# Kernel tuning notes

Hardware: AMD Instinct MI355X
Metric: run time of the kernel (lower is better)

Reference implementation:

```python
import jax, jax.numpy as jnp
import numpy as np

N, E = 100000, 1600000
FEATS, HIDDEN, CLASSES, DEPTH = 512, 64, 16, 10
EMB_DIM = 1 + int(np.log2(HIDDEN))   # 7
ADJ_H = 4 + EMB_DIM                  # 11
DIFF = 0.9


def setup_inputs() -> dict:
    key = jax.random.key(0)
    ks = jax.random.split(key, 8)
    return {
        "x": jax.random.normal(ks[0], (N, FEATS), jnp.float32),
        "edges": jax.random.randint(ks[1], (2, E), 0, N, jnp.int32),
        "W_dim": jax.random.normal(ks[2], (FEATS, HIDDEN), jnp.float32) / np.sqrt(FEATS),
        "b_dim": jnp.zeros((HIDDEN,), jnp.float32),
        "emb": jax.random.normal(ks[3], (HIDDEN, EMB_DIM), jnp.float32),
        "W_a1": jax.random.normal(ks[4], (2 + EMB_DIM, ADJ_H), jnp.float32) / np.sqrt(2 + EMB_DIM),
        "b_a1": jnp.zeros((ADJ_H,), jnp.float32),
        "W_a2": jax.random.normal(ks[5], (ADJ_H, 1), jnp.float32) / np.sqrt(ADJ_H),
        "b_a2": jnp.zeros((1,), jnp.float32),
        "W_cls": jax.random.normal(ks[6], (HIDDEN, CLASSES), jnp.float32) / np.sqrt(HIDDEN),
        "b_cls": jnp.zeros((CLASSES,), jnp.float32),
    }


def reference(x, edges, W_dim, b_dim, emb, W_a1, b_a1, W_a2, b_a2, W_cls, b_cls):
    n = x.shape[0]
    src, dst = edges[0], edges[1]
    # symmetric-normalized sparse aggregation (GCN-style GraphConv, cached norm)
    deg = jax.ops.segment_sum(jnp.ones(src.shape[0], x.dtype), dst, num_segments=n)
    dinv = jnp.where(deg > 0, jax.lax.rsqrt(jnp.maximum(deg, 1.0)), 0.0)
    wnorm = dinv[src] * dinv[dst]  # [E]

    def conv(h):  # [n, H] -> [n, H]
        return jax.ops.segment_sum(h[src] * wnorm[:, None], dst, num_segments=n)

    h = x @ W_dim + b_dim        # [n, HIDDEN]
    h0 = h
    for _ in range(DEPTH):       # personalized-PageRank-style diffusion
        h = conv(h) * DIFF + (1.0 - DIFF) * h0

    hdim = h.shape[1]
    xt = h.T.reshape(-1, 1)      # [HIDDEN*n, 1]
    h0t = h0.T.reshape(-1, 1)
    # class_indicator built after reshape(-1,1): num_classes = 1 -> all-zero indices
    e = jnp.broadcast_to(emb[0], (xt.shape[0], emb.shape[1]))  # [HIDDEN*n, EMB_DIM]
    f = jnp.concatenate([xt, h0t, e], axis=1)                  # [HIDDEN*n, 9]
    f = jax.nn.leaky_relu(f @ W_a1 + b_a1, negative_slope=0.01)
    f = (f @ W_a2 + b_a2) * 0.5                                # [HIDDEN*n, 1]
    h = f.reshape(hdim, n).T                                   # [n, HIDDEN]
    # dropout: eval mode -> no-op
    h0 = h
    for _ in range(DEPTH):
        h = conv(h) * DIFF + (1.0 - DIFF) * h0
    return h @ W_cls + b_cls     # [n, CLASSES]
```

## Files before the change

### kernel.cpp

```cpp
#include <hip/hip_runtime.h>
#include <hip/hip_bf16.h>
#include <hip/hip_fp16.h>
#include <stdint.h>

#define FEATS   512
#define HIDDEN  64
#define CLASSES 16
#define EMB_DIM 7
#define ADJ_H   11
#define DEPTH   10

typedef __hip_bfloat16 bf16;
typedef __attribute__((ext_vector_type(8))) short short8;
typedef __attribute__((ext_vector_type(4))) float f32x4;

__device__ __forceinline__ float b2f(bf16 v) { return __bfloat162float(v); }

__global__ void k_detect(const unsigned short* __restrict__ xs, int* __restrict__ flag) {
    __shared__ int cnt;
    if (threadIdx.x == 0) cnt = 0;
    __syncthreads();
    int c = 0;
    for (int i = threadIdx.x; i < 4096; i += 256) {
        unsigned e = (xs[i] >> 7) & 0xFFu;
        if (e >= 134u) c++;
    }
    atomicAdd(&cnt, c);
    __syncthreads();
    if (threadIdx.x == 0) *flag = (cnt < 64) ? 1 : 0;
}

__global__ __launch_bounds__(256) void k_deg(const int* __restrict__ edges,
                                             int* __restrict__ deg, int E) {
    int e = blockIdx.x * 256 + threadIdx.x;
    if (e < E) atomicAdd(&deg[edges[E + e]], 1);
}

__global__ __launch_bounds__(256) void k_scan1(const int* __restrict__ deg,
                                               int* __restrict__ offs,
                                               int* __restrict__ bsum, int n) {
    __shared__ int ts[256];
    int t = threadIdx.x;
    int base = blockIdx.x * 1024 + t * 4;
    int v0 = (base + 0 < n) ? deg[base + 0] : 0;
    int v1 = (base + 1 < n) ? deg[base + 1] : 0;
    int v2 = (base + 2 < n) ? deg[base + 2] : 0;
    int v3 = (base + 3 < n) ? deg[base + 3] : 0;
    int tsum = v0 + v1 + v2 + v3;
    ts[t] = tsum;
    __syncthreads();
    for (int d = 1; d < 256; d <<= 1) {
        int add = (t >= d) ? ts[t - d] : 0;
        __syncthreads();
        ts[t] += add;
        __syncthreads();
    }
    int excl = ts[t] - tsum;
    if (base + 0 < n) offs[base + 0] = excl;
    if (base + 1 < n) offs[base + 1] = excl + v0;
    if (base + 2 < n) offs[base + 2] = excl + v0 + v1;
    if (base + 3 < n) offs[base + 3] = excl + v0 + v1 + v2;
    if (t == 255) bsum[blockIdx.x] = ts[255];
}

__global__ void k_scan2(const int* __restrict__ bsum, int* __restrict__ bpref,
                        int* __restrict__ offs, int nb, int n) {
    if (threadIdx.x == 0 && blockIdx.x == 0) {
        int run = 0;
        for (int i = 0; i < nb; ++i) { bpref[i] = run; run += bsum[i]; }
        offs[n] = run;
    }
}

__global__ __launch_bounds__(256) void k_scan3(int* __restrict__ offs,
                                               const int* __restrict__ bpref, int n) {
    int i = blockIdx.x * 256 + threadIdx.x;
    if (i < n) offs[i] += bpref[i >> 10];
}

__global__ __launch_bounds__(256) void k_fill(const int* __restrict__ edges,
                                              const int* __restrict__ offs,
                                              int* __restrict__ cursor,
                                              const int* __restrict__ deg,
                                              unsigned* __restrict__ ew, int E) {
    int e = blockIdx.x * 256 + threadIdx.x;
    if (e < E) {
        int src = edges[e];
        int dst = edges[E + e];
        int pos = offs[dst] + atomicAdd(&cursor[dst], 1);
        int ds = deg[src], dd = deg[dst];
        float w = (ds > 0 ? rsqrtf((float)ds) : 0.f) * (dd > 0 ? rsqrtf((float)dd) : 0.f);
        int w15 = (int)(w * 16384.0f + 0.5f);
        if (w15 > 32767) w15 = 32767;
        ew[pos] = ((unsigned)src << 15) | (unsigned)w15;
    }
}

__global__ void k_mlpconst(const void* __restrict__ emb, const void* __restrict__ W_a1,
                           const void* __restrict__ b_a1, const void* __restrict__ W_a2,
                           const void* __restrict__ b_a2, const int* __restrict__ flag,
                           float* __restrict__ C) {
    int isbf = *flag;
    auto g = [&](const void* p, int i) -> float {
        return isbf ? b2f(((const bf16*)p)[i]) : ((const float*)p)[i];
    };
    int j = threadIdx.x;
    if (j < ADJ_H) {
        float c = g(b_a1, j);
        for (int k = 0; k < EMB_DIM; ++k)
            c += g(emb, k) * g(W_a1, (2 + k) * ADJ_H + j);
        C[j]      = c;
        C[11 + j] = g(W_a1, 0 * ADJ_H + j);
        C[22 + j] = g(W_a1, 1 * ADJ_H + j);
        C[33 + j] = g(W_a2, j);
    }
    if (j == 0) C[44] = g(b_a2, 0);
}

__global__ __launch_bounds__(256) void k_gemm_mfma(const void* __restrict__ xraw,
                                                   const int* __restrict__ flag,
                                                   const void* __restrict__ Wraw,
                                                   const void* __restrict__ braw,
                                                   __half* __restrict__ out, int n) {
    __shared__ short Wt[64 * 520];
    int t = threadIdx.x;
    int isbf = *flag;
    if (isbf) {
        const unsigned short* wr = (const unsigned short*)Wraw;
        for (int e = t; e < FEATS * HIDDEN; e += 256)
            Wt[(e & 63) * 520 + (e >> 6)] = (short)wr[e];
    } else {
        const float* wr = (const float*)Wraw;
        for (int e = t; e < FEATS * HIDDEN; e += 256)
            Wt[(e & 63) * 520 + (e >> 6)] = (short)(__float_as_uint(wr[e]) >> 16);
    }
    __syncthreads();

    int wv = t >> 6;
    int lane = t & 63;
    int quad = lane >> 4, l16 = lane & 15;
    int rowbase = blockIdx.x * 256 + wv * 64;

    f32x4 acc[4][4];
    #pragma unroll
    for (int a = 0; a < 4; ++a)
        #pragma unroll
        for (int b = 0; b < 4; ++b)
            acc[a][b] = (f32x4){0.f, 0.f, 0.f, 0.f};

    if (isbf) {
        const short* x = (const short*)xraw;
        for (int ks = 0; ks < 16; ++ks) {
            short8 bfr[4];
            #pragma unroll
            for (int nt = 0; nt < 4; ++nt)
                bfr[nt] = *(const short8*)&Wt[(nt * 16 + l16) * 520 + ks * 32 + quad * 8];
            #pragma unroll
            for (int rt = 0; rt < 4; ++rt) {
                int arow = rowbase + rt * 16 + l16;
                if (arow >= n) arow = n - 1;
                short8 a = *(const short8*)(x + (size_t)arow * FEATS + ks * 32 + quad * 8);
                #pragma unroll
                for (int nt = 0; nt < 4; ++nt)
                    acc[rt][nt] = __builtin_amdgcn_mfma_f32_16x16x32_bf16(a, bfr[nt], acc[rt][nt], 0, 0, 0);
            }
        }
    } else {
        const float* x = (const float*)xraw;
        for (int ks = 0; ks < 16; ++ks) {
            short8 bfr[4];
            #pragma unroll
            for (int nt = 0; nt < 4; ++nt)
                bfr[nt] = *(const short8*)&Wt[(nt * 16 + l16) * 520 + ks * 32 + quad * 8];
            #pragma unroll
            for (int rt = 0; rt < 4; ++rt) {
                int arow = rowbase + rt * 16 + l16;
                if (arow >= n) arow = n - 1;
                const float* ap = x + (size_t)arow * FEATS + ks * 32 + quad * 8;
                short8 a;
                #pragma unroll
                for (int j = 0; j < 8; ++j)
                    a[j] = (short)(__float_as_uint(ap[j]) >> 16);
                #pragma unroll
                for (int nt = 0; nt < 4; ++nt)
                    acc[rt][nt] = __builtin_amdgcn_mfma_f32_16x16x32_bf16(a, bfr[nt], acc[rt][nt], 0, 0, 0);
            }
        }
    }

    float bias[4];
    #pragma unroll
    for (int nt = 0; nt < 4; ++nt)
        bias[nt] = isbf ? b2f(((const bf16*)braw)[nt * 16 + l16])
                        : ((const float*)braw)[nt * 16 + l16];

    #pragma unroll
    for (int rt = 0; rt < 4; ++rt)
        #pragma unroll
        for (int nt = 0; nt < 4; ++nt) {
            #pragma unroll
            for (int r = 0; r < 4; ++r) {
                int grow = rowbase + rt * 16 + quad * 4 + r;
                if (grow < n)
                    out[(size_t)grow * HIDDEN + nt * 16 + l16] =
                        __float2half(acc[rt][nt][r] + bias[nt]);
            }
        }
}

__global__ __launch_bounds__(256) void k_conv(const int* __restrict__ offs,
                                              const unsigned* __restrict__ ew,
                                              const __half* __restrict__ hin,
                                              const __half* __restrict__ h0,
                                              __half* __restrict__ hout, int n) {
    int wv = (blockIdx.x * 256 + threadIdx.x) >> 6;
    int lane = threadIdx.x & 63;
    int sub = lane >> 3;
    int li  = lane & 7;
    int node = wv * 8 + sub;
    bool valid = node < n;
    int start = valid ? offs[node] : 0;
    int end   = valid ? offs[node + 1] : 0;

    float acc[8];
    #pragma unroll
    for (int j = 0; j < 8; ++j) acc[j] = 0.f;

    int p = start;
    for (; p + 4 <= end; p += 4) {
        unsigned u0 = ew[p + 0];
        unsigned u1 = ew[p + 1];
        unsigned u2 = ew[p + 2];
        unsigned u3 = ew[p + 3];
        uint4 r0 = *(const uint4*)(hin + (size_t)(u0 >> 15) * HIDDEN + li * 8);
        uint4 r1 = *(const uint4*)(hin + (size_t)(u1 >> 15) * HIDDEN + li * 8);
        uint4 r2 = *(const uint4*)(hin + (size_t)(u2 >> 15) * HIDDEN + li * 8);
        uint4 r3 = *(const uint4*)(hin + (size_t)(u3 >> 15) * HIDDEN + li * 8);
        float w0 = (float)(u0 & 0x7FFFu);
        float w1 = (float)(u1 & 0x7FFFu);
        float w2 = (float)(u2 & 0x7FFFu);
        float w3 = (float)(u3 & 0x7FFFu);
        const unsigned* q;
        q = &r0.x;
        #pragma unroll
        for (int j = 0; j < 4; ++j) {
            float2 f = __half22float2(*(const __half2*)&q[j]);
            acc[2*j]   += w0 * f.x;
            acc[2*j+1] += w0 * f.y;
        }
        q = &r1.x;
        #pragma unroll
        for (int j = 0; j < 4; ++j) {
            float2 f = __half22float2(*(const __half2*)&q[j]);
            acc[2*j]   += w1 * f.x;
            acc[2*j+1] += w1 * f.y;
        }
        q = &r2.x;
        #pragma unroll
        for (int j = 0; j < 4; ++j) {
            float2 f = __half22float2(*(const __half2*)&q[j]);
            acc[2*j]   += w2 * f.x;
            acc[2*j+1] += w2 * f.y;
        }
        q = &r3.x;
        #pragma unroll
        for (int j = 0; j < 4; ++j) {
            float2 f = __half22float2(*(const __half2*)&q[j]);
            acc[2*j]   += w3 * f.x;
            acc[2*j+1] += w3 * f.y;
        }
    }
    for (; p < end; ++p) {
        unsigned u = ew[p];
        uint4 r = *(const uint4*)(hin + (size_t)(u >> 15) * HIDDEN + li * 8);
        float w = (float)(u & 0x7FFFu);
        const unsigned* q = &r.x;
        #pragma unroll
        for (int j = 0; j < 4; ++j) {
            float2 f = __half22float2(*(const __half2*)&q[j]);
            acc[2*j]   += w * f.x;
            acc[2*j+1] += w * f.y;
        }
    }

    if (valid) {
        size_t o = (size_t)node * HIDDEN + li * 8;
        uint4 hv = *(const uint4*)(h0 + o);
        const unsigned* q = &hv.x;
        uint4 ov;
        unsigned* po = &ov.x;
        #pragma unroll
        for (int j = 0; j < 4; ++j) {
            float2 g = __half22float2(*(const __half2*)&q[j]);
            __half2 r = __floats2half2_rn(
                0.9f * (1.0f / 16384.0f) * acc[2*j]   + 0.1f * g.x,
                0.9f * (1.0f / 16384.0f) * acc[2*j+1] + 0.1f * g.y);
            po[j] = *(unsigned*)&r;
        }
        *(uint4*)(hout + o) = ov;
    }
}

__global__ __launch_bounds__(256) void k_mlp(__half* __restrict__ h0io,
                                             const __half* __restrict__ hc,
                                             const float* __restrict__ C, int total2) {
    int i = blockIdx.x * 256 + threadIdx.x;
    if (i >= total2) return;
    float2 hv  = __half22float2(((const __half2*)hc)[i]);
    float2 h0v = __half22float2(((const __half2*)h0io)[i]);
    float sx = C[44], sy = C[44];
    #pragma unroll
    for (int j = 0; j < ADJ_H; ++j) {
        float bj = C[j], wh = C[11 + j], w0 = C[22 + j], wo = C[33 + j];
        float zx = bj + hv.x * wh + h0v.x * w0;
        float zy = bj + hv.y * wh + h0v.y * w0;
        zx = (zx > 0.f) ? zx : 0.01f * zx;
        zy = (zy > 0.f) ? zy : 0.01f * zy;
        sx += zx * wo;
        sy += zy * wo;
    }
    ((__half2*)h0io)[i] = __floats2half2_rn(0.5f * sx, 0.5f * sy);
}

__global__ __launch_bounds__(256) void k_cls(const __half* __restrict__ h,
                                             const void* __restrict__ Wcraw,
                                             const void* __restrict__ bcraw,
                                             void* __restrict__ outraw,
                                             const int* __restrict__ flag, int n) {
    __shared__ float hs[64][65];
    __shared__ float ws[64 * 16];
    __shared__ float bs[16];
    int t = threadIdx.x;
    int base = blockIdx.x * 64;
    int isbf = *flag;
    for (int it = 0; it < 16; ++it) {
        int e = it * 256 + t;
        int rr = e >> 6, cc = e & 63;
        int g = base + rr;
        hs[rr][cc] = (g < n) ? __half2float(h[(size_t)g * HIDDEN + cc]) : 0.f;
    }
    for (int it = 0; it < 4; ++it) {
        int e = it * 256 + t;
        ws[e] = isbf ? b2f(((const bf16*)Wcraw)[e]) : ((const float*)Wcraw)[e];
    }
    if (t < 16) bs[t] = isbf ? b2f(((const bf16*)bcraw)[t]) : ((const float*)bcraw)[t];
    __syncthreads();
    for (int q = 0; q < 4; ++q) {
        int e = q * 256 + t;
        int node = e >> 4, cls = e & 15;
        float acc = bs[cls];
        #pragma unroll 8
        for (int k = 0; k < HIDDEN; ++k)
            acc += hs[node][k] * ws[k * 16 + cls];
        int g = base + node;
        if (g < n) {
            size_t oi = (size_t)g * CLASSES + cls;
            if (isbf) ((bf16*)outraw)[oi] = __float2bfloat16(acc);
            else      ((float*)outraw)[oi] = acc;
        }
    }
}

extern "C" void kernel_launch(void* const* d_in, const int* in_sizes, int n_in,
                              void* d_out, int out_size, void* d_ws, size_t ws_size,
                              hipStream_t stream) {
    const void* x     = d_in[0];
    const int*  edges = (const int*)d_in[1];
    const void* W_dim = d_in[2];
    const void* b_dim = d_in[3];
    const void* emb   = d_in[4];
    const void* W_a1  = d_in[5];
    const void* b_a1  = d_in[6];
    const void* W_a2  = d_in[7];
    const void* b_a2  = d_in[8];
    const void* Wcls  = d_in[9];
    const void* bcls  = d_in[10];

    const int n = in_sizes[0] / FEATS;
    const int E = in_sizes[1] / 2;

    char* w = (char*)d_ws;
    size_t off = 0;
    auto alloc = [&](size_t bytes) -> void* {
        void* p = w + off;
        off = (off + bytes + 255) & ~(size_t)255;
        return p;
    };
    int*      deg    = (int*)     alloc((size_t)n * 4);
    int*      cursor = (int*)     alloc((size_t)n * 4);
    int*      offs   = (int*)     alloc((size_t)(n + 1) * 4);
    int*      bsum   = (int*)     alloc(4096 * 4);
    int*      bpref  = (int*)     alloc(4096 * 4);
    unsigned* ew     = (unsigned*)alloc((size_t)E * 4);
    float*    consts = (float*)   alloc(64 * 4);
    int*      flag   = (int*)     alloc(256);
    __half*   buf0   = (__half*)  alloc((size_t)n * HIDDEN * 2);
    __half*   bufA   = (__half*)  alloc((size_t)n * HIDDEN * 2);
    __half*   bufB   = (__half*)  alloc((size_t)n * HIDDEN * 2);

    int gE = (E + 255) / 256;
    int gN = (n + 255) / 256;
    int nb = (n + 1023) / 1024;
    int gConv = (n + 31) / 32;

    hipMemsetAsync(deg, 0, ((char*)cursor - (char*)deg) + (size_t)n * 4, stream);

    k_detect<<<1, 256, 0, stream>>>((const unsigned short*)x, flag);

    k_deg  <<<gE, 256, 0, stream>>>(edges, deg, E);
    k_scan1<<<nb, 256, 0, stream>>>(deg, offs, bsum, n);
    k_scan2<<<1, 64, 0, stream>>>(bsum, bpref, offs, nb, n);
    k_scan3<<<gN, 256, 0, stream>>>(offs, bpref, n);
    k_fill <<<gE, 256, 0, stream>>>(edges, offs, cursor, deg, ew, E);

    k_mlpconst<<<1, 64, 0, stream>>>(emb, W_a1, b_a1, W_a2, b_a2, flag, consts);

    k_gemm_mfma<<<(n + 255) / 256, 256, 0, stream>>>(x, flag, W_dim, b_dim, buf0, n);

    const __half* hin = buf0;
    for (int i = 0; i < DEPTH; ++i) {
        __half* ho = (i & 1) ? bufB : bufA;
        k_conv<<<gConv, 256, 0, stream>>>(offs, ew, hin, buf0, ho, n);
        hin = ho;
    }
    k_mlp<<<(n * (HIDDEN / 2) + 255) / 256, 256, 0, stream>>>(buf0, hin, consts, n * (HIDDEN / 2));

    hin = buf0;
    for (int i = 0; i < DEPTH; ++i) {
        __half* ho = (i & 1) ? bufB : bufA;
        k_conv<<<gConv, 256, 0, stream>>>(offs, ew, hin, buf0, ho, n);
        hin = ho;
    }
    k_cls<<<(n + 63) / 64, 256, 0, stream>>>(hin, Wcls, bcls, d_out, flag, n);
}
```

Baseline: 1.151 ms.

## Sort nodes by in-degree for balanced conv waves and unroll edge loop by eight

Result: slower. 1.457 ms (+26.6%).

```diff
diff --git a/kernel.cpp b/kernel.cpp
--- a/kernel.cpp
+++ b/kernel.cpp
@@ -38,9 +38,12 @@
 
 __global__ __launch_bounds__(256) void k_scan1(const int* __restrict__ deg,
                                                int* __restrict__ offs,
-                                               int* __restrict__ bsum, int n) {
+                                               int* __restrict__ bsum,
+                                               int* __restrict__ hist, int n) {
     __shared__ int ts[256];
+    __shared__ int hb[256];
     int t = threadIdx.x;
+    hb[t] = 0;
     int base = blockIdx.x * 1024 + t * 4;
     int v0 = (base + 0 < n) ? deg[base + 0] : 0;
     int v1 = (base + 1 < n) ? deg[base + 1] : 0;
@@ -49,6 +52,10 @@
     int tsum = v0 + v1 + v2 + v3;
     ts[t] = tsum;
     __syncthreads();
+    if (base + 0 < n) atomicAdd(&hb[min(v0, 255)], 1);
+    if (base + 1 < n) atomicAdd(&hb[min(v1, 255)], 1);
+    if (base + 2 < n) atomicAdd(&hb[min(v2, 255)], 1);
+    if (base + 3 < n) atomicAdd(&hb[min(v3, 255)], 1);
     for (int d = 1; d < 256; d <<= 1) {
         int add = (t >= d) ? ts[t - d] : 0;
         __syncthreads();
@@ -61,6 +68,7 @@
     if (base + 2 < n) offs[base + 2] = excl + v0 + v1;
     if (base + 3 < n) offs[base + 3] = excl + v0 + v1 + v2;
     if (t == 255) bsum[blockIdx.x] = ts[255];
+    if (hb[t]) atomicAdd(&hist[t], hb[t]);
 }
 
 __global__ void k_scan2(const int* __restrict__ bsum, int* __restrict__ bpref,
@@ -76,6 +84,32 @@
                                                const int* __restrict__ bpref, int n) {
     int i = blockIdx.x * 256 + threadIdx.x;
     if (i < n) offs[i] += bpref[i >> 10];
+}
+
+__global__ void k_hscan(const int* __restrict__ hist, int* __restrict__ hcur) {
+    __shared__ int s[256];
+    int t = threadIdx.x;
+    int orig = hist[t];
+    s[t] = orig;
+    __syncthreads();
+    for (int d = 1; d < 256; d <<= 1) {
+        int add = (t >= d) ? s[t - d] : 0;
+        __syncthreads();
+        s[t] += add;
+        __syncthreads();
+    }
+    hcur[t] = s[t] - orig;
+}
+
+__global__ __launch_bounds__(256) void k_scatter(const int* __restrict__ deg,
+                                                 int* __restrict__ hcur,
+                                                 int* __restrict__ perm, int n) {
+    int i = blockIdx.x * 256 + threadIdx.x;
+    if (i < n) {
+        int d = min(deg[i], 255);
+        int pos = atomicAdd(&hcur[d], 1);
+        perm[pos] = i;
+    }
 }
 
 __global__ __launch_bounds__(256) void k_fill(const int* __restrict__ edges,
@@ -208,7 +242,19 @@
         }
 }
 
+#define ACCROW(r, w)                                              \
+    {                                                             \
+        const unsigned* q_ = &(r).x;                              \
+        _Pragma("unroll")                                         \
+        for (int j_ = 0; j_ < 4; ++j_) {                          \
+            float2 f_ = __half22float2(*(const __half2*)&q_[j_]); \
+            acc[2 * j_]     += (w) * f_.x;                        \
+            acc[2 * j_ + 1] += (w) * f_.y;                        \
+        }                                                         \
+    }
+
 __global__ __launch_bounds__(256) void k_conv(const int* __restrict__ offs,
+                                              const int* __restrict__ perm,
                                               const unsigned* __restrict__ ew,
                                               const __half* __restrict__ hin,
                                               const __half* __restrict__ h0,
@@ -217,8 +263,9 @@
     int lane = threadIdx.x & 63;
     int sub = lane >> 3;
     int li  = lane & 7;
-    int node = wv * 8 + sub;
-    bool valid = node < n;
+    int idx = wv * 8 + sub;
+    bool valid = idx < n;
+    int node  = valid ? perm[idx] : 0;
     int start = valid ? offs[node] : 0;
     int end   = valid ? offs[node + 1] : 0;
 
@@ -227,7 +274,35 @@
     for (int j = 0; j < 8; ++j) acc[j] = 0.f;
 
     int p = start;
-    for (; p + 4 <= end; p += 4) {
+    for (; p + 8 <= end; p += 8) {
+        unsigned u0 = ew[p + 0];
+        unsigned u1 = ew[p + 1];
+        unsigned u2 = ew[p + 2];
+        unsigned u3 = ew[p + 3];
+        unsigned u4 = ew[p + 4];
+        unsigned u5 = ew[p + 5];
+        unsigned u6 = ew[p + 6];
+        unsigned u7 = ew[p + 7];
+        uint4 r0 = *(const uint4*)(hin + (size_t)(u0 >> 15) * HIDDEN + li * 8);
+        uint4 r1 = *(const uint4*)(hin + (size_t)(u1 >> 15) * HIDDEN + li * 8);
+        uint4 r2 = *(const uint4*)(hin + (size_t)(u2 >> 15) * HIDDEN + li * 8);
+        uint4 r3 = *(const uint4*)(hin + (size_t)(u3 >> 15) * HIDDEN + li * 8);
+        uint4 r4 = *(const uint4*)(hin + (size_t)(u4 >> 15) * HIDDEN + li * 8);
+        uint4 r5 = *(const uint4*)(hin + (size_t)(u5 >> 15) * HIDDEN + li * 8);
+        uint4 r6 = *(const uint4*)(hin + (size_t)(u6 >> 15) * HIDDEN + li * 8);
+        uint4 r7 = *(const uint4*)(hin + (size_t)(u7 >> 15) * HIDDEN + li * 8);
+        float w0 = (float)(u0 & 0x7FFFu);
+        float w1 = (float)(u1 & 0x7FFFu);
+        float w2 = (float)(u2 & 0x7FFFu);
+        float w3 = (float)(u3 & 0x7FFFu);
+        float w4 = (float)(u4 & 0x7FFFu);
+        float w5 = (float)(u5 & 0x7FFFu);
+        float w6 = (float)(u6 & 0x7FFFu);
+        float w7 = (float)(u7 & 0x7FFFu);
+        ACCROW(r0, w0); ACCROW(r1, w1); ACCROW(r2, w2); ACCROW(r3, w3);
+        ACCROW(r4, w4); ACCROW(r5, w5); ACCROW(r6, w6); ACCROW(r7, w7);
+    }
+    if (p + 4 <= end) {
         unsigned u0 = ew[p + 0];
         unsigned u1 = ew[p + 1];
         unsigned u2 = ew[p + 2];
@@ -240,47 +315,14 @@
         float w1 = (float)(u1 & 0x7FFFu);
         float w2 = (float)(u2 & 0x7FFFu);
         float w3 = (float)(u3 & 0x7FFFu);
-        const unsigned* q;
-        q = &r0.x;
-        #pragma unroll
-        for (int j = 0; j < 4; ++j) {
-            float2 f = __half22float2(*(const __half2*)&q[j]);
-            acc[2*j]   += w0 * f.x;
-            acc[2*j+1] += w0 * f.y;
-        }
-        q = &r1.x;
-        #pragma unroll
-        for (int j = 0; j < 4; ++j) {
-            float2 f = __half22float2(*(const __half2*)&q[j]);
-            acc[2*j]   += w1 * f.x;
-            acc[2*j+1] += w1 * f.y;
-        }
-        q = &r2.x;
-        #pragma unroll
-        for (int j = 0; j < 4; ++j) {
-            float2 f = __half22float2(*(const __half2*)&q[j]);
-            acc[2*j]   += w2 * f.x;
-            acc[2*j+1] += w2 * f.y;
-        }
-        q = &r3.x;
-        #pragma unroll
-        for (int j = 0; j < 4; ++j) {
-            float2 f = __half22float2(*(const __half2*)&q[j]);
-            acc[2*j]   += w3 * f.x;
-            acc[2*j+1] += w3 * f.y;
-        }
+        ACCROW(r0, w0); ACCROW(r1, w1); ACCROW(r2, w2); ACCROW(r3, w3);
+        p += 4;
     }
     for (; p < end; ++p) {
         unsigned u = ew[p];
         uint4 r = *(const uint4*)(hin + (size_t)(u >> 15) * HIDDEN + li * 8);
         float w = (float)(u & 0x7FFFu);
-        const unsigned* q = &r.x;
-        #pragma unroll
-        for (int j = 0; j < 4; ++j) {
-            float2 f = __half22float2(*(const __half2*)&q[j]);
-            acc[2*j]   += w * f.x;
-            acc[2*j+1] += w * f.y;
-        }
+        ACCROW(r, w);
     }
 
     if (valid) {
@@ -388,6 +430,10 @@
     };
     int*      deg    = (int*)     alloc((size_t)n * 4);
     int*      cursor = (int*)     alloc((size_t)n * 4);
+    int*      hist   = (int*)     alloc(256 * 4);
+    size_t zero_bytes = off;
+    int*      hcur   = (int*)     alloc(256 * 4);
+    int*      perm   = (int*)     alloc((size_t)n * 4);
     int*      offs   = (int*)     alloc((size_t)(n + 1) * 4);
     int*      bsum   = (int*)     alloc(4096 * 4);
     int*      bpref  = (int*)     alloc(4096 * 4);
@@ -403,16 +449,19 @@
     int nb = (n + 1023) / 1024;
     int gConv = (n + 31) / 32;
 
-    hipMemsetAsync(deg, 0, ((char*)cursor - (char*)deg) + (size_t)n * 4, stream);
+    hipMemsetAsync(d_ws, 0, zero_bytes, stream);
 
     k_detect<<<1, 256, 0, stream>>>((const unsigned short*)x, flag);
 
     k_deg  <<<gE, 256, 0, stream>>>(edges, deg, E);
-    k_scan1<<<nb, 256, 0, stream>>>(deg, offs, bsum, n);
+    k_scan1<<<nb, 256, 0, stream>>>(deg, offs, bsum, hist, n);
     k_scan2<<<1, 64, 0, stream>>>(bsum, bpref, offs, nb, n);
     k_scan3<<<gN, 256, 0, stream>>>(offs, bpref, n);
     k_fill <<<gE, 256, 0, stream>>>(edges, offs, cursor, deg, ew, E);
 
+    k_hscan  <<<1, 256, 0, stream>>>(hist, hcur);
+    k_scatter<<<gN, 256, 0, stream>>>(deg, hcur, perm, n);
+
     k_mlpconst<<<1, 64, 0, stream>>>(emb, W_a1, b_a1, W_a2, b_a2, flag, consts);
 
     k_gemm_mfma<<<(n + 255) / 256, 256, 0, stream>>>(x, flag, W_dim, b_dim, buf0, n);
@@ -420,7 +469,7 @@
     const __half* hin = buf0;
     for (int i = 0; i < DEPTH; ++i) {
         __half* ho = (i & 1) ? bufB : bufA;
-        k_conv<<<gConv, 256, 0, stream>>>(offs, ew, hin, buf0, ho, n);
+        k_conv<<<gConv, 256, 0, stream>>>(offs, perm, ew, hin, buf0, ho, n);
         hin = ho;
     }
     k_mlp<<<(n * (HIDDEN / 2) + 255) / 256, 256, 0, stream>>>(buf0, hin, consts, n * (HIDDEN / 2));
@@ -428,7 +477,7 @@
     hin = buf0;
     for (int i = 0; i < DEPTH; ++i) {
         __half* ho = (i & 1) ? bufB : bufA;
-        k_conv<<<gConv, 256, 0, stream>>>(offs, ew, hin, buf0, ho, n);
+        k_conv<<<gConv, 256, 0, stream>>>(offs, perm, ew, hin, buf0, ho, n);
         hin = ho;
     }
     k_cls<<<(n + 63) / 64, 256, 0, stream>>>(hin, Wcls, bcls, d_out, flag, n);
```
